# Performance work log

Hardware: AMD Instinct MI355X
Metric: run time of the kernel (lower is better)

Reference implementation:

```python
import jax, jax.numpy as jnp
import numpy as np

# DETR-style matcher constants
COST_CLASS, COST_BBOX, COST_GIOU = 1.0, 5.0, 2.0
BS, Q, NUM_CLASSES, T = 16, 900, 92, 100  # 16 images, 900 queries, 100 targets/image


def setup_inputs() -> dict:
    key = jax.random.key(0)
    k1, k2, k3, k4, k5, k6 = jax.random.split(key, 6)
    pred_logits = jax.random.normal(k1, (BS, Q, NUM_CLASSES), dtype=jnp.float32)
    # predicted boxes in cxcywh, valid sizes
    cxcy = jax.random.uniform(k2, (BS, Q, 2), dtype=jnp.float32)
    wh = jax.random.uniform(k3, (BS, Q, 2), dtype=jnp.float32) * 0.5 + 0.01
    pred_boxes = jnp.concatenate([cxcy, wh], axis=-1)
    # targets: ids and xyxy boxes, concatenated over the batch (T per image)
    tgt_ids = jax.random.randint(k4, (BS * T,), 0, NUM_CLASSES, dtype=jnp.int64)
    tc = jax.random.uniform(k5, (BS * T, 2), dtype=jnp.float32)
    tw = jax.random.uniform(k6, (BS * T, 2), dtype=jnp.float32) * 0.5 + 0.01
    tgt_bbox = jnp.concatenate([tc - tw / 2.0, tc + tw / 2.0], axis=-1)  # xyxy
    return {"pred_logits": pred_logits, "pred_boxes": pred_boxes,
            "tgt_ids": tgt_ids, "tgt_bbox": tgt_bbox}


def box_cxcywh_to_xyxy(b):
    c, s = b[..., :2], b[..., 2:]
    return jnp.concatenate([c - s / 2.0, c + s / 2.0], axis=-1)


def box_xyxy_to_cxcywh(b):
    return jnp.concatenate([(b[..., :2] + b[..., 2:]) / 2.0,
                            b[..., 2:] - b[..., :2]], axis=-1)


def generalized_box_iou(a, b):
    # a: [N,4] xyxy, b: [M,4] xyxy -> [N,M]
    area_a = (a[:, 2] - a[:, 0]) * (a[:, 3] - a[:, 1])
    area_b = (b[:, 2] - b[:, 0]) * (b[:, 3] - b[:, 1])
    lt = jnp.maximum(a[:, None, :2], b[None, :, :2])
    rb = jnp.minimum(a[:, None, 2:], b[None, :, 2:])
    wh = jnp.clip(rb - lt, 0.0)
    inter = wh[..., 0] * wh[..., 1]
    union = area_a[:, None] + area_b[None, :] - inter
    iou = inter / union
    lt_c = jnp.minimum(a[:, None, :2], b[None, :, :2])
    rb_c = jnp.maximum(a[:, None, 2:], b[None, :, 2:])
    wh_c = jnp.clip(rb_c - lt_c, 0.0)
    area_c = wh_c[..., 0] * wh_c[..., 1]
    return iou - (area_c - union) / area_c


def _cost_matrix(pred_logits, pred_boxes, tgt_ids, tgt_bbox):
    bs, q, nc = pred_logits.shape
    out_prob = jax.nn.softmax(pred_logits.reshape(-1, nc), axis=-1)  # [bs*Q, C]
    out_bbox = pred_boxes.reshape(-1, 4)                              # [bs*Q, 4] cxcywh
    cost_class = -out_prob[:, tgt_ids]                                # [bs*Q, M]
    cost_bbox = jnp.abs(out_bbox[:, None, :] -
                        box_xyxy_to_cxcywh(tgt_bbox)[None, :, :]).sum(-1)  # L1 cdist
    cost_giou = -generalized_box_iou(box_cxcywh_to_xyxy(out_bbox), tgt_bbox)
    C = COST_BBOX * cost_bbox + COST_CLASS * cost_class + COST_GIOU * cost_giou
    return C.reshape(bs, q, -1)


_cost_matrix_jit = jax.jit(_cost_matrix)


def _lsa(cost):
    # Jonker-Volgenant shortest augmenting path; cost [n, m] with n <= m.
    # Returns col assignment for each row (minimizing total cost).
    n, m = cost.shape
    u = np.zeros(n + 1)
    v = np.zeros(m + 1)
    p = np.zeros(m + 1, dtype=np.int64)   # p[j] = row (1-indexed) assigned to col j
    way = np.zeros(m + 1, dtype=np.int64)
    cpad = np.zeros((n + 1, m + 1))
    cpad[1:, 1:] = cost
    for i in range(1, n + 1):
        p[0] = i
        j0 = 0
        minv = np.full(m + 1, np.inf)
        used = np.zeros(m + 1, dtype=bool)
        while True:
            used[j0] = True
            i0 = p[j0]
            idx = np.nonzero(~used)[0]
            idx = idx[idx > 0]
            cur = cpad[i0, idx] - u[i0] - v[idx]
            better = cur < minv[idx]
            minv[idx[better]] = cur[better]
            way[idx[better]] = j0
            k = np.argmin(minv[idx])
            delta = minv[idx[k]]
            j1 = idx[k]
            u[p[used]] += delta
            v[used] -= delta
            minv[~used] -= delta
            j0 = j1
            if p[j0] == 0:
                break
        while j0:
            j1 = way[j0]
            p[j0] = p[j1]
            j0 = j1
    ans = np.zeros(n, dtype=np.int64)
    for j in range(1, m + 1):
        if p[j] > 0:
            ans[p[j] - 1] = j - 1
    return ans


def reference(pred_logits, pred_boxes, tgt_ids, tgt_bbox):
    C = _cost_matrix_jit(pred_logits, pred_boxes, tgt_ids, tgt_bbox)  # [BS, Q, BS*T]
    Cn = np.asarray(C)
    rows = np.zeros((BS, T), dtype=np.int64)
    cols = np.zeros((BS, T), dtype=np.int64)
    for i in range(BS):  # per-image serial assignment, as in the original
        c = Cn[i, :, i * T:(i + 1) * T]          # [Q, T], Q >= T
        pred_for_tgt = _lsa(c.T)                 # [T]: target j -> query row
        order = np.argsort(pred_for_tgt)         # scipy returns sorted row indices
        rows[i] = pred_for_tgt[order]
        cols[i] = order
    return C, jnp.asarray(rows), jnp.asarray(cols)
```

## Files before the change

kernel.cpp:

```cpp
#include <hip/hip_runtime.h>
#include <math.h>

#define BS 16
#define QN 900
#define NC 92
#define TN 100
#define NQ (BS * QN)
#define NT (BS * TN)
#define C_ELEMS ((size_t)NQ * NT)
#define NK 15
#define F4N 225
#define NS 16
#define ARR_CAP 300
#define UNM_CAP 416
#define SLICE_F4 (TN * F4N)

template<int CTRL>
__device__ __forceinline__ float dpp_fmin_step(float x) {
    int xi = __float_as_int(x);
    int yi = __builtin_amdgcn_update_dpp(xi, xi, CTRL, 0xF, 0xF, false);
    return fminf(x, __int_as_float(yi));
}
__device__ __forceinline__ float wave_fmin_to63(float x) {
    x = dpp_fmin_step<0x111>(x);
    x = dpp_fmin_step<0x112>(x);
    x = dpp_fmin_step<0x114>(x);
    x = dpp_fmin_step<0x118>(x);
    x = dpp_fmin_step<0x142>(x);
    x = dpp_fmin_step<0x143>(x);
    return x;
}
__device__ __forceinline__ float readlane63_f(float x) {
    return __uint_as_float(__builtin_amdgcn_readlane(__float_as_uint(x), 63));
}

template<int CTRL>
__device__ __forceinline__ void dpp_fmin2_step(float& a1, float& a2) {
    int o1i = __builtin_amdgcn_update_dpp(__float_as_int(a1), __float_as_int(a1),
                                          CTRL, 0xF, 0xF, false);
    int o2i = __builtin_amdgcn_update_dpp(__float_as_int(a2), __float_as_int(a2),
                                          CTRL, 0xF, 0xF, false);
    float o1 = __int_as_float(o1i), o2 = __int_as_float(o2i);
    float hi = fmaxf(a1, o1);
    a1 = fminf(a1, o1);
    a2 = fminf(hi, fminf(a2, o2));
}
__device__ __forceinline__ void wave_fmin2_to63(float& a1, float& a2) {
    dpp_fmin2_step<0x111>(a1, a2);
    dpp_fmin2_step<0x112>(a1, a2);
    dpp_fmin2_step<0x114>(a1, a2);
    dpp_fmin2_step<0x118>(a1, a2);
    dpp_fmin2_step<0x142>(a1, a2);
    dpp_fmin2_step<0x143>(a1, a2);
}

__device__ __forceinline__ int slot_of(int c) { return ((c >> 8) << 2) | (c & 3); }
__device__ __forceinline__ int owner_of(int c) { return (c >> 2) & 63; }

__device__ __forceinline__ int read_colreg16(const int arr[NS], int c) {
    int s = slot_of(c);
    int v = 0;
    #pragma unroll
    for (int k = 0; k < NS; ++k) if (k == s) v = arr[k];
    return __builtin_amdgcn_readlane(v, owner_of(c));
}

__device__ __forceinline__ float readrow_u(float u0, float u1, int r) {
    return __uint_as_float(__builtin_amdgcn_readlane(
        __float_as_uint(r < 64 ? u0 : u1), r & 63));
}

__device__ __forceinline__ void issue_row(const float4* cst4, int irow, int lane,
        float4& r0, float4& r1, float4& r2, float4& r3) {
    const float4* cr = cst4 + (size_t)(irow - 1) * F4N;
    r0 = cr[lane];
    r1 = cr[lane + 64];
    r2 = cr[lane + 128];
    if (lane < 33) r3 = cr[lane + 192];
}

__device__ __forceinline__ float cost_entry(
        float px2, float py2, float pw, float ph,
        float ax0, float ay0, float ax1, float ay1,
        float area_a, float base_cls, float4 tb) {
    float tw = tb.z - tb.x;
    float th = tb.w - tb.y;
    float area_b = tw * th;
    float sx = px2 - (tb.x + tb.z);
    float sy = py2 - (tb.y + tb.w);
    float dw = pw - tw;
    float dh = ph - th;
    float cb = fmaf(0.5f, fabsf(sx), fabsf(dw)) + fmaf(0.5f, fabsf(sy), fabsf(dh));
    float ltx = fmaxf(ax0, tb.x), lty = fmaxf(ay0, tb.y);
    float rbx = fminf(ax1, tb.z), rby = fminf(ay1, tb.w);
    float iw = fmaxf(rbx - ltx, 0.0f), ih = fmaxf(rby - lty, 0.0f);
    float inter = iw * ih;
    float uni = (area_a + area_b) - inter;
    float cx0 = fminf(ax0, tb.x), cy0 = fminf(ay0, tb.y);
    float cx1 = fmaxf(ax1, tb.z), cy1 = fmaxf(ay1, tb.w);
    float area_c = (cx1 - cx0) * (cy1 - cy0);
    float num = fmaf(uni, uni, inter * area_c);
    float r   = __builtin_amdgcn_rcpf(uni * area_c);
    return fmaf(-2.0f, num * r, fmaf(5.0f, cb, base_cls));
}

__global__ __launch_bounds__(256) void softmax_cost_kernel(
        const float* __restrict__ logits,
        const float4* __restrict__ pboxes,
        const int4* __restrict__ tids4,
        const float4* __restrict__ tbox,
        float* __restrict__ C,
        float* __restrict__ cost_t) {
    __shared__ float shp[4][NC];
    int wid = threadIdx.x >> 6;
    int lane = threadIdx.x & 63;
    int q = blockIdx.x * 4 + wid;
    const float* row = logits + (size_t)q * NC;
    float x0 = (lane < NC) ? row[lane] : -INFINITY;
    float x1 = (lane + 64 < NC) ? row[lane + 64] : -INFINITY;
    float m = fmaxf(x0, x1);
    for (int off = 32; off; off >>= 1) m = fmaxf(m, __shfl_xor(m, off));
    float e0 = (lane < NC) ? expf(x0 - m) : 0.0f;
    float e1 = (lane + 64 < NC) ? expf(x1 - m) : 0.0f;
    float s = e0 + e1;
    for (int off = 32; off; off >>= 1) s += __shfl_xor(s, off);
    float rs = __builtin_amdgcn_rcpf(s);
    if (lane < NC) shp[wid][lane] = fmaf(-e0, rs, 2.0f);
    if (lane + 64 < NC) shp[wid][lane + 64] = fmaf(-e1, rs, 2.0f);
    __syncthreads();
    float4 pb = pboxes[q];
    float hx = pb.z * 0.5f, hy = pb.w * 0.5f;
    float ax0 = pb.x - hx, ay0 = pb.y - hy;
    float ax1 = pb.x + hx, ay1 = pb.y + hy;
    float area_a = pb.z * pb.w;
    float px2 = pb.x + pb.x, py2 = pb.y + pb.y;
    int b = q / QN;
    int diag_lo = b * 25;
    float* ctb = cost_t + (size_t)b * TN * QN + (q - b * QN);
    float4* crow4 = (float4*)(C + (size_t)q * NT);
    #pragma unroll 2
    for (int t4 = lane; t4 < NT / 4; t4 += 64) {
        int4 id = tids4[t4];
        int t = t4 * 4;
        float4 r;
        r.x = cost_entry(px2, py2, pb.z, pb.w, ax0, ay0, ax1, ay1, area_a,
                         shp[wid][id.x], tbox[t]);
        r.y = cost_entry(px2, py2, pb.z, pb.w, ax0, ay0, ax1, ay1, area_a,
                         shp[wid][id.y], tbox[t + 1]);
        r.z = cost_entry(px2, py2, pb.z, pb.w, ax0, ay0, ax1, ay1, area_a,
                         shp[wid][id.z], tbox[t + 2]);
        r.w = cost_entry(px2, py2, pb.z, pb.w, ax0, ay0, ax1, ay1, area_a,
                         shp[wid][id.w], tbox[t + 3]);
        crow4[t4] = r;
        int tl = t4 - diag_lo;
        if ((unsigned)tl < 25u) {
            float* dst = ctb + (size_t)(4 * tl) * QN;
            dst[0]        = r.x;
            dst[QN]       = r.y;
            dst[2 * QN]   = r.z;
            dst[3 * QN]   = r.w;
        }
    }
}

__global__ __launch_bounds__(256) void rowmin_kernel(
        const float* __restrict__ cost_t,
        unsigned long long* __restrict__ rm) {
    int wid = threadIdx.x >> 6;
    int lane = threadIdx.x & 63;
    int t = blockIdx.x * 4 + wid;
    const float4* cr = (const float4*)(cost_t + (size_t)t * QN);
    float4 a0 = cr[lane];
    float4 a1 = cr[lane + 64];
    float4 a2 = cr[lane + 128];
    float4 a3 = make_float4(INFINITY, INFINITY, INFINITY, INFINITY);
    if (lane < 33) a3 = cr[lane + 192];
    float dd[NS];
    dd[0]  = a0.x; dd[1]  = a0.y; dd[2]  = a0.z; dd[3]  = a0.w;
    dd[4]  = a1.x; dd[5]  = a1.y; dd[6]  = a1.z; dd[7]  = a1.w;
    dd[8]  = a2.x; dd[9]  = a2.y; dd[10] = a2.z; dd[11] = a2.w;
    dd[12] = a3.x; dd[13] = a3.y; dd[14] = a3.z; dd[15] = a3.w;
    float l1 = INFINITY; int ls = 0;
    #pragma unroll
    for (int s = 0; s < NS; ++s) {
        bool lt = dd[s] < l1;
        ls = lt ? s : ls;
        l1 = lt ? dd[s] : l1;
    }
    float mv = readlane63_f(wave_fmin_to63(l1));
    unsigned long long eq = __ballot(l1 == mv);
    int wl = __ffsll(eq) - 1;
    int myq = (lane << 2) + ((ls >> 2) << 8) + (ls & 3);
    int ma = __builtin_amdgcn_readlane(myq, wl);
    if (lane == 0)
        rm[t] = ((unsigned long long)__float_as_uint(mv) << 32) | (unsigned)ma;
}

__global__ __launch_bounds__(256, 1) void lsa_kernel(
        const float* __restrict__ cost_t,
        const unsigned long long* __restrict__ rm,
        float* __restrict__ out) {
    int b = blockIdx.x;
    int wv = threadIdx.x >> 6;
    int lane = threadIdx.x & 63;
    const float4* cst4 = (const float4*)(cost_t + (size_t)b * TN * QN);
    __shared__ float u_s[TN];
    __shared__ int p_s[QN];
    __shared__ int unm[UNM_CAP];
    __shared__ int dij[UNM_CAP];

    if (wv != 0) {
        int start = (wv - 1) * (SLICE_F4 / 3);
        int end   = (wv == 3) ? SLICE_F4 : wv * (SLICE_F4 / 3);
        float acc = 0.0f;
        #pragma unroll 4
        for (int i = start + lane; i < end; i += 64) {
            float4 x = cst4[i];
            acc += (x.x + x.y) + (x.z + x.w);
        }
        asm volatile("" :: "v"(acc));
        return;
    }

    float v_r[NS], dist_r[NS];
    int way_r[NS], pcol_r[NS];
    float4 pre0, pre1, pre2, pre3 = make_float4(0.f, 0.f, 0.f, 0.f);
    float4 rc0, rc1, rc2, rc3 = make_float4(0.f, 0.f, 0.f, 0.f);
    const bool v3 = (lane < 33);

    #pragma unroll
    for (int s = 0; s < NS; ++s) v_r[s] = 0.0f;
    for (int j = lane; j < QN; j += 64) p_s[j] = 0x7fffffff;

    int arg0 = 0, arg1 = 0;
    float u0 = 0.0f, u1 = 0.0f;
    {
        unsigned long long k0 = rm[b * TN + lane];
        u0 = __uint_as_float((unsigned)(k0 >> 32));
        arg0 = (int)(k0 & 0xffffffffu);
        u_s[lane] = u0;
        if (lane + 64 < TN) {
            unsigned long long k1 = rm[b * TN + lane + 64];
            u1 = __uint_as_float((unsigned)(k1 >> 32));
            arg1 = (int)(k1 & 0xffffffffu);
            u_s[lane + 64] = u1;
        }
    }

    atomicMin(&p_s[arg0], lane + 1);
    if (lane + 64 < TN) atomicMin(&p_s[arg1], lane + 65);
    int nunm = 0;
    {
        bool um0 = (p_s[arg0] != lane + 1);
        unsigned long long m0 = __ballot(um0);
        if (um0) unm[__popcll(m0 & ((1ull << lane) - 1ull))] = lane + 1;
        nunm = __popcll(m0);
        bool um1 = (lane + 64 < TN) && (p_s[arg1] != lane + 65);
        unsigned long long m1 = __ballot(um1);
        if (um1) unm[nunm + __popcll(m1 & ((1ull << lane) - 1ull))] = lane + 65;
        nunm += __popcll(m1);
    }
    #pragma unroll
    for (int s = 0; s < NS; ++s) {
        int f = lane + ((s >> 2) << 6);
        int c = (f << 2) | (s & 3);
        pcol_r[s] = 0;
        if (f < F4N) { int pv = p_s[c]; pcol_r[s] = (pv == 0x7fffffff) ? 0 : pv; }
    }

    int qhead = 0, qtail = nunm, dij_n = 0, pops = 0;
    if (qhead < qtail) issue_row(cst4, unm[0], lane, pre0, pre1, pre2, pre3);
    while (qhead < qtail) {
        int i_cur = unm[qhead++];
        ++pops;
        if (pops > ARR_CAP) {
            if (lane == 0) dij[dij_n] = i_cur;
            dij_n++;
            continue;
        }
        float dd[NS];
        dd[0]  = pre0.x - v_r[0];  dd[1]  = pre0.y - v_r[1];
        dd[2]  = pre0.z - v_r[2];  dd[3]  = pre0.w - v_r[3];
        dd[4]  = pre1.x - v_r[4];  dd[5]  = pre1.y - v_r[5];
        dd[6]  = pre1.z - v_r[6];  dd[7]  = pre1.w - v_r[7];
        dd[8]  = pre2.x - v_r[8];  dd[9]  = pre2.y - v_r[9];
        dd[10] = pre2.z - v_r[10]; dd[11] = pre2.w - v_r[11];
        if (v3) {
            dd[12] = pre3.x - v_r[12]; dd[13] = pre3.y - v_r[13];
            dd[14] = pre3.z - v_r[14]; dd[15] = pre3.w - v_r[15];
        } else {
            dd[12] = INFINITY; dd[13] = INFINITY;
            dd[14] = INFINITY; dd[15] = INFINITY;
        }
        bool pf = false;
        if (qhead < qtail) { issue_row(cst4, unm[qhead], lane, pre0, pre1, pre2, pre3); pf = true; }
        float a1[NS], a2[NS]; int ai[NS], ap[NS];
        #pragma unroll
        for (int s = 0; s < NS; ++s) {
            a1[s] = dd[s]; a2[s] = INFINITY; ai[s] = s; ap[s] = pcol_r[s];
        }
        #pragma unroll
        for (int n = 8; n >= 1; n >>= 1) {
            #pragma unroll
            for (int i = 0; i < n; ++i) {
                bool tk = a1[2 * i + 1] < a1[2 * i];
                float m1 = tk ? a1[2 * i + 1] : a1[2 * i];
                float ms = tk ? fminf(a1[2 * i], a2[2 * i + 1])
                              : fminf(a1[2 * i + 1], a2[2 * i]);
                a1[i] = m1; a2[i] = ms;
                ai[i] = tk ? ai[2 * i + 1] : ai[2 * i];
                ap[i] = tk ? ap[2 * i + 1] : ap[2 * i];
            }
        }
        float lmin = a1[0];
        int ls = ai[0];
        int pv = ap[0];
        int myj = (lane << 2) + ((ls >> 2) << 8) + (ls & 3);
        float w1 = a1[0], w2 = a2[0];
        wave_fmin2_to63(w1, w2);
        float d1 = readlane63_f(w1);
        float d2 = readlane63_f(w2);
        unsigned long long eqm = __ballot(lmin == d1);
        int wl = __ffsll(eqm) - 1;
        int j1 = __builtin_amdgcn_readlane(myj, wl);
        int i0 = __builtin_amdgcn_readlane(pv, wl);
        bool take = (d1 < d2) || (i0 == 0);
        if (take) {
            if (i0 != 0) {
                if (!pf) issue_row(cst4, i0, lane, pre0, pre1, pre2, pre3);
                if (lane == 0) unm[qtail] = i0;
                qtail++;
            }
            int s1 = slot_of(j1), ow = owner_of(j1);
            float dv_ = d2 - d1;
            #pragma unroll
            for (int s = 0; s < NS; ++s)
                if (s == s1 && lane == ow) { v_r[s] -= dv_; pcol_r[s] = i_cur; }
            if (lane == 0) u_s[i_cur - 1] = d2;
        } else {
            if (lane == 0) { u_s[i_cur - 1] = d2; dij[dij_n] = i_cur; }
            dij_n++;
        }
    }
    u0 = u_s[lane];
    if (lane + 64 < TN) u1 = u_s[lane + 64];

    if (dij_n > 0) issue_row(cst4, dij[0], lane, pre0, pre1, pre2, pre3);

    for (int ui = 0; ui < dij_n; ++ui) {
        int i_cur = dij[ui];
        unsigned used_mask = 0;
        float uic = readrow_u(u0, u1, i_cur - 1);
        #pragma unroll
        for (int s = 0; s < NS; ++s) way_r[s] = -1;
        dist_r[0]  = (pre0.x - uic) - v_r[0];
        dist_r[1]  = (pre0.y - uic) - v_r[1];
        dist_r[2]  = (pre0.z - uic) - v_r[2];
        dist_r[3]  = (pre0.w - uic) - v_r[3];
        dist_r[4]  = (pre1.x - uic) - v_r[4];
        dist_r[5]  = (pre1.y - uic) - v_r[5];
        dist_r[6]  = (pre1.z - uic) - v_r[6];
        dist_r[7]  = (pre1.w - uic) - v_r[7];
        dist_r[8]  = (pre2.x - uic) - v_r[8];
        dist_r[9]  = (pre2.y - uic) - v_r[9];
        dist_r[10] = (pre2.z - uic) - v_r[10];
        dist_r[11] = (pre2.w - uic) - v_r[11];
        if (v3) {
            dist_r[12] = (pre3.x - uic) - v_r[12];
            dist_r[13] = (pre3.y - uic) - v_r[13];
            dist_r[14] = (pre3.z - uic) - v_r[14];
            dist_r[15] = (pre3.w - uic) - v_r[15];
        } else {
            dist_r[12] = INFINITY; dist_r[13] = INFINITY;
            dist_r[14] = INFINITY; dist_r[15] = INFINITY;
        }
        if (ui + 1 < dij_n) issue_row(cst4, dij[ui + 1], lane, pre0, pre1, pre2, pre3);

        float dfin; int jfree;
        while (true) {
            float dv[NS]; int dk[NS]; int pc[NS];
            #pragma unroll
            for (int s = 0; s < NS; ++s) {
                dv[s] = (used_mask & (1u << s)) ? INFINITY : dist_r[s];
                dk[s] = s;
                pc[s] = pcol_r[s];
            }
            #pragma unroll
            for (int n = 8; n >= 1; n >>= 1) {
                #pragma unroll
                for (int i = 0; i < n; ++i) {
                    bool tk = dv[2 * i + 1] < dv[2 * i];
                    dv[i] = tk ? dv[2 * i + 1] : dv[2 * i];
                    dk[i] = tk ? dk[2 * i + 1] : dk[2 * i];
                    pc[i] = tk ? pc[2 * i + 1] : pc[2 * i];
                }
            }
            float lv = dv[0];
            int s0 = dk[0];
            int li = (lane << 2) + ((s0 >> 2) << 8) + (s0 & 3);
            float dmin = readlane63_f(wave_fmin_to63(lv));
            unsigned long long eq = __ballot(lv == dmin);
            int winner = __ffsll(eq) - 1;
            int j1 = __builtin_amdgcn_readlane(li, winner);
            int pj1 = __builtin_amdgcn_readlane(pc[0], winner);
            if (pj1 == 0) { dfin = dmin; jfree = j1; break; }
            {
                int s1 = slot_of(j1), ow1 = owner_of(j1);
                if (lane == ow1) used_mask |= (1u << s1);
            }
            issue_row(cst4, pj1, lane, rc0, rc1, rc2, rc3);
            float ui0 = readrow_u(u0, u1, pj1 - 1);
            float off = dmin - ui0;
            #define RELAX(S, V) \
                if (!(used_mask & (1u << (S)))) { \
                    float nd = ((V) - v_r[S]) + off; \
                    if (nd < dist_r[S]) { dist_r[S] = nd; way_r[S] = j1; } }
            RELAX(0,  rc0.x) RELAX(1,  rc0.y) RELAX(2,  rc0.z) RELAX(3,  rc0.w)
            RELAX(4,  rc1.x) RELAX(5,  rc1.y) RELAX(6,  rc1.z) RELAX(7,  rc1.w)
            RELAX(8,  rc2.x) RELAX(9,  rc2.y) RELAX(10, rc2.z) RELAX(11, rc2.w)
            if (v3) {
                RELAX(12, rc3.x) RELAX(13, rc3.y) RELAX(14, rc3.z) RELAX(15, rc3.w)
            }
            #undef RELAX
        }
        #pragma unroll
        for (int s = 0; s < NS; ++s) {
            if (used_mask & (1u << s)) {
                float a = dfin - dist_r[s];
                v_r[s] -= a;
                u_s[pcol_r[s] - 1] += a;
            }
        }
        if (lane == 0) u_s[i_cur - 1] += dfin;
        u0 = u_s[lane];
        if (lane + 64 < TN) u1 = u_s[lane + 64];
        {
            int jj = jfree;
            while (true) {
                int wj = read_colreg16(way_r, jj);
                int pn = (wj < 0) ? i_cur : read_colreg16(pcol_r, wj);
                int sj = slot_of(jj), ow = owner_of(jj);
                #pragma unroll
                for (int s = 0; s < NS; ++s)
                    if (s == sj && lane == ow) pcol_r[s] = pn;
                if (wj < 0) break;
                jj = wj;
            }
        }
    }

    #pragma unroll
    for (int s = 0; s < NS; ++s) {
        int f = lane + ((s >> 2) << 6);
        int c = (f << 2) | (s & 3);
        if (f < F4N) p_s[c] = pcol_r[s];
    }
    float* rows = out + C_ELEMS + (size_t)b * TN;
    float* cols = out + C_ELEMS + (size_t)BS * TN + (size_t)b * TN;
    int base = 0;
    #pragma unroll
    for (int k = 0; k < NK; ++k) {
        int c = lane + (k << 6);
        int pv = (c < QN) ? p_s[c] : 0;
        unsigned long long mask = __ballot(pv > 0);
        if (pv > 0) {
            int rank = base + __popcll(mask & ((1ull << lane) - 1ull));
            rows[rank] = (float)c;
            cols[rank] = (float)(pv - 1);
        }
        base += __popcll(mask);
    }
}

extern "C" void kernel_launch(void* const* d_in, const int* in_sizes, int n_in,
                              void* d_out, int out_size, void* d_ws, size_t ws_size,
                              hipStream_t stream) {
    const float* logits = (const float*)d_in[0];
    const float4* pboxes = (const float4*)d_in[1];
    const int* tids = (const int*)d_in[2];
    const float4* tbox = (const float4*)d_in[3];
    float* out = (float*)d_out;

    float* cost_t = (float*)d_ws;
    unsigned long long* rm =
        (unsigned long long*)(cost_t + (size_t)BS * TN * QN);

    softmax_cost_kernel<<<NQ / 4, 256, 0, stream>>>(logits, pboxes, (const int4*)tids, tbox, out, cost_t);
    rowmin_kernel<<<NT / 4, 256, 0, stream>>>(cost_t, rm);
    lsa_kernel<<<BS, 256, 0, stream>>>(cost_t, rm, out);
}
```

Baseline: 167.4 us.

## Split diagonal cost computation and overlap full cost matrix write with LSA

The first kernel now computes only the per-image diagonal cost blocks needed by the assignment solver, writing the transposed slice. The full cost-matrix output is written by extra blocks added to the LSA launch, so the large C write runs concurrently with the serial per-image assignment instead of before it. The trade-off is that softmax and diagonal costs are computed twice, and the extra blocks compete with the 16 LSA blocks for memory bandwidth. Whether LSA blocks get scheduled first also depends on block dispatch order.

```diff
diff --git a/kernel.cpp b/kernel.cpp
--- a/kernel.cpp
+++ b/kernel.cpp
@@ -104,17 +104,9 @@
     return fmaf(-2.0f, num * r, fmaf(5.0f, cb, base_cls));
 }
 
-__global__ __launch_bounds__(256) void softmax_cost_kernel(
-        const float* __restrict__ logits,
-        const float4* __restrict__ pboxes,
-        const int4* __restrict__ tids4,
-        const float4* __restrict__ tbox,
-        float* __restrict__ C,
-        float* __restrict__ cost_t) {
-    __shared__ float shp[4][NC];
-    int wid = threadIdx.x >> 6;
-    int lane = threadIdx.x & 63;
-    int q = blockIdx.x * 4 + wid;
+__device__ __forceinline__ void softmax_to_lds(
+        const float* __restrict__ logits, int q, int wid, int lane,
+        float shp[4][NC]) {
     const float* row = logits + (size_t)q * NC;
     float x0 = (lane < NC) ? row[lane] : -INFINITY;
     float x1 = (lane + 64 < NC) ? row[lane + 64] : -INFINITY;
@@ -127,6 +119,19 @@
     float rs = __builtin_amdgcn_rcpf(s);
     if (lane < NC) shp[wid][lane] = fmaf(-e0, rs, 2.0f);
     if (lane + 64 < NC) shp[wid][lane + 64] = fmaf(-e1, rs, 2.0f);
+}
+
+__global__ __launch_bounds__(256) void diag_cost_kernel(
+        const float* __restrict__ logits,
+        const float4* __restrict__ pboxes,
+        const int4* __restrict__ tids4,
+        const float4* __restrict__ tbox,
+        float* __restrict__ cost_t) {
+    __shared__ float shp[4][NC];
+    int wid = threadIdx.x >> 6;
+    int lane = threadIdx.x & 63;
+    int q = blockIdx.x * 4 + wid;
+    softmax_to_lds(logits, q, wid, lane, shp);
     __syncthreads();
     float4 pb = pboxes[q];
     float hx = pb.z * 0.5f, hy = pb.w * 0.5f;
@@ -137,9 +142,8 @@
     int b = q / QN;
     int diag_lo = b * 25;
     float* ctb = cost_t + (size_t)b * TN * QN + (q - b * QN);
-    float4* crow4 = (float4*)(C + (size_t)q * NT);
-    #pragma unroll 2
-    for (int t4 = lane; t4 < NT / 4; t4 += 64) {
+    if (lane < 25) {
+        int t4 = diag_lo + lane;
         int4 id = tids4[t4];
         int t = t4 * 4;
         float4 r;
@@ -151,15 +155,11 @@
                          shp[wid][id.z], tbox[t + 2]);
         r.w = cost_entry(px2, py2, pb.z, pb.w, ax0, ay0, ax1, ay1, area_a,
                          shp[wid][id.w], tbox[t + 3]);
-        crow4[t4] = r;
-        int tl = t4 - diag_lo;
-        if ((unsigned)tl < 25u) {
-            float* dst = ctb + (size_t)(4 * tl) * QN;
-            dst[0]        = r.x;
-            dst[QN]       = r.y;
-            dst[2 * QN]   = r.z;
-            dst[3 * QN]   = r.w;
-        }
+        float* dst = ctb + (size_t)(4 * lane) * QN;
+        dst[0]        = r.x;
+        dst[QN]       = r.y;
+        dst[2 * QN]   = r.z;
+        dst[3 * QN]   = r.w;
     }
 }
 
@@ -196,18 +196,55 @@
         rm[t] = ((unsigned long long)__float_as_uint(mv) << 32) | (unsigned)ma;
 }
 
-__global__ __launch_bounds__(256, 1) void lsa_kernel(
+__global__ __launch_bounds__(256, 1) void fused_cost_lsa_kernel(
+        const float* __restrict__ logits,
+        const float4* __restrict__ pboxes,
+        const int4* __restrict__ tids4,
+        const float4* __restrict__ tbox,
         const float* __restrict__ cost_t,
         const unsigned long long* __restrict__ rm,
         float* __restrict__ out) {
+    __shared__ float shp[4][NC];
+    __shared__ float u_s[TN];
+    __shared__ int p_s[QN];
+    __shared__ int unm[UNM_CAP];
+    __shared__ int dij[UNM_CAP];
+
+    if (blockIdx.x >= 16) {
+        int wid = threadIdx.x >> 6;
+        int lane = threadIdx.x & 63;
+        int q = (blockIdx.x - 16) * 4 + wid;
+        softmax_to_lds(logits, q, wid, lane, shp);
+        __syncthreads();
+        float4 pb = pboxes[q];
+        float hx = pb.z * 0.5f, hy = pb.w * 0.5f;
+        float ax0 = pb.x - hx, ay0 = pb.y - hy;
+        float ax1 = pb.x + hx, ay1 = pb.y + hy;
+        float area_a = pb.z * pb.w;
+        float px2 = pb.x + pb.x, py2 = pb.y + pb.y;
+        float4* crow4 = (float4*)(out + (size_t)q * NT);
+        #pragma unroll 2
+        for (int t4 = lane; t4 < NT / 4; t4 += 64) {
+            int4 id = tids4[t4];
+            int t = t4 * 4;
+            float4 r;
+            r.x = cost_entry(px2, py2, pb.z, pb.w, ax0, ay0, ax1, ay1, area_a,
+                             shp[wid][id.x], tbox[t]);
+            r.y = cost_entry(px2, py2, pb.z, pb.w, ax0, ay0, ax1, ay1, area_a,
+                             shp[wid][id.y], tbox[t + 1]);
+            r.z = cost_entry(px2, py2, pb.z, pb.w, ax0, ay0, ax1, ay1, area_a,
+                             shp[wid][id.z], tbox[t + 2]);
+            r.w = cost_entry(px2, py2, pb.z, pb.w, ax0, ay0, ax1, ay1, area_a,
+                             shp[wid][id.w], tbox[t + 3]);
+            crow4[t4] = r;
+        }
+        return;
+    }
+
     int b = blockIdx.x;
     int wv = threadIdx.x >> 6;
     int lane = threadIdx.x & 63;
     const float4* cst4 = (const float4*)(cost_t + (size_t)b * TN * QN);
-    __shared__ float u_s[TN];
-    __shared__ int p_s[QN];
-    __shared__ int unm[UNM_CAP];
-    __shared__ int dij[UNM_CAP];
 
     if (wv != 0) {
         int start = (wv - 1) * (SLICE_F4 / 3);
@@ -485,7 +522,8 @@
     unsigned long long* rm =
         (unsigned long long*)(cost_t + (size_t)BS * TN * QN);
 
-    softmax_cost_kernel<<<NQ / 4, 256, 0, stream>>>(logits, pboxes, (const int4*)tids, tbox, out, cost_t);
+    diag_cost_kernel<<<NQ / 4, 256, 0, stream>>>(logits, pboxes, (const int4*)tids, tbox, cost_t);
     rowmin_kernel<<<NT / 4, 256, 0, stream>>>(cost_t, rm);
-    lsa_kernel<<<BS, 256, 0, stream>>>(cost_t, rm, out);
-}
+    fused_cost_lsa_kernel<<<16 + NQ / 4, 256, 0, stream>>>(
+        logits, pboxes, (const int4*)tids, tbox, cost_t, rm, out);
+}
```

Result: faster. 145.6 us (-13.0%).
